# Performance work log

Hardware: AMD Instinct MI355X
Metric: run time of the kernel (lower is better)

## Reference

```python
import jax, jax.numpy as jnp
import numpy as np
jax.config.update("jax_enable_x64", True)

B, S, V, W, M = 64, 32, 512, 2048, 8
EOS, PAD, MSK = 0, 1, 2
DELTA_IMAG_CLAMP = 35.0  # standard tmm overflow guard on exp(+Im(delta))


def setup_inputs() -> dict:
    key = jax.random.key(0)
    ks = jax.random.split(key, 6)
    stacks = jax.random.uniform(ks[0], (B, S, V), dtype=jnp.float32)
    wl_tensor = (400.0 + 700.0 * jax.random.uniform(ks[1], (W,), dtype=jnp.float32))  # nm
    theta = jnp.zeros((1,), dtype=jnp.float32)  # normal incidence
    nk_real = 1.5 + 2.5 * jax.random.uniform(ks[2], (M, W), dtype=jnp.float64)
    nk_imag = 0.5 * jax.random.uniform(ks[3], (M, W), dtype=jnp.float64)
    thickness = 5.0 + 195.0 * jax.random.uniform(ks[4], (V,), dtype=jnp.float64)
    thickness = thickness.at[jnp.array([EOS, PAD, MSK])].set(0.0)  # special tokens -> substrate, 0 nm
    mat_idx_table = jax.random.randint(ks[5], (V,), 0, M, dtype=jnp.int32)
    sub_idx = jnp.array(0, dtype=jnp.int32)
    return dict(stacks=stacks, wl_tensor=wl_tensor, theta=theta,
                nk_real=nk_real, nk_imag=nk_imag, thickness=thickness,
                mat_idx_table=mat_idx_table, sub_idx=sub_idx,
                eos=EOS, pad=PAD, msk=MSK)


def _coh_tmm_s(n, t, th0, lam):
    """Coherent TMM, s-pol. n:[B,L,W] complex128, t:[B,L] complex128 (front/back inf),
    th0 scalar, lam:[W]. Returns R,T [B,W] float."""
    n0 = n[:, :1, :]
    th = jnp.arcsin(n0 * jnp.sin(th0) / n)           # Snell, complex arcsin [B,L,W]
    cos_th = jnp.cos(th)
    kz = 2.0 * jnp.pi * n * cos_th / lam[None, None, :]
    delta = kz[:, 1:-1, :] * t[:, 1:-1, None]        # inner layers only [B,S,W]
    delta = delta.real + 1j * jnp.minimum(delta.imag, DELTA_IMAG_CLAMP)
    f = n * cos_th                                    # [B,L,W]
    f1, f2 = f[:, :-1, :], f[:, 1:, :]
    r = (f1 - f2) / (f1 + f2)                         # interface Fresnel r [B,L-1,W]
    tt = 2.0 * f1 / (f1 + f2)
    # Mtilde = ([[1,r0],[r0,1]]/t0) @ prod_j (diag(e^{-i d_j}, e^{+i d_j}) @ [[1,rj],[rj,1]]/tj)
    a = 1.0 / tt[:, 0]
    b = r[:, 0] / tt[:, 0]
    c = b
    d = a

    def step(carry, xs):
        a, b, c, d = carry
        dlt, rj, tj = xs                              # each [B,W]
        P = jnp.exp(-1j * dlt)
        Q = jnp.exp(1j * dlt)
        inv_t = 1.0 / tj
        a2 = (a * P + b * Q * rj) * inv_t
        b2 = (a * P * rj + b * Q) * inv_t
        c2 = (c * P + d * Q * rj) * inv_t
        d2 = (c * P * rj + d * Q) * inv_t
        return (a2, b2, c2, d2), None

    xs = (jnp.moveaxis(delta, 1, 0), jnp.moveaxis(r[:, 1:], 1, 0), jnp.moveaxis(tt[:, 1:], 1, 0))
    (a, b, c, d), _ = jax.lax.scan(step, (a, b, c, d), xs)
    r_amp = c / a
    t_amp = 1.0 / a
    R = jnp.abs(r_amp) ** 2
    T = jnp.abs(t_amp) ** 2 * (f[:, -1].real / f[:, 0].real)
    return R, T


def reference(stacks, wl_tensor, theta, nk_real, nk_imag, thickness, mat_idx_table, sub_idx, eos, pad, msk):
    nk_table = nk_real + 1j * nk_imag                 # [M,W] complex128
    th_c = thickness.astype(jnp.complex128)           # [V]
    nk_per_token = nk_table[mat_idx_table]            # [V,W]
    # zero out special-token probabilities and renormalize
    p = stacks.at[:, :, jnp.array([eos, pad, msk])].set(0.0)
    Z = p.sum(axis=-1, keepdims=True)
    p_norm = jnp.where(Z > 0, p / jnp.maximum(Z, 1e-8), p)
    p_c = p_norm.astype(jnp.complex128)
    n_base = jnp.einsum('bsv,vw->bsw', p_c, nk_per_token)  # soft nk gather
    t_base = p_c @ th_c                                     # [B,S]
    is_zero = Z[..., 0] <= 0
    n_base = jnp.where(is_zero[..., None], nk_table[sub_idx][None, None, :], n_base)
    t_base = jnp.where(is_zero, jnp.zeros((), dtype=t_base.dtype), t_base)
    # soft EOS survival mask
    p_eos = jnp.clip(stacks[..., eos], 0.0, 1.0)
    survival = jnp.cumprod(1.0 - p_eos + 1e-12, axis=1)
    active = jnp.concatenate([jnp.ones_like(survival[:, :1]), survival[:, :-1]], axis=1)
    t_base = t_base * active.astype(t_base.dtype)
    Bb, Ss, Ww = n_base.shape
    one = jnp.ones((Bb, 1, Ww), dtype=n_base.dtype)
    inf_t = jnp.full((Bb, 1), jnp.inf, dtype=t_base.dtype)
    n_tensor = jnp.concatenate([one, n_base, one], axis=1)     # [B,S+2,W]
    t_tensor = jnp.concatenate([inf_t, t_base, inf_t], axis=1)  # [B,S+2]
    th0 = theta[0].astype(jnp.float64)
    lam = wl_tensor.astype(jnp.float64)
    R, T = _coh_tmm_s(n_tensor, t_tensor, th0, lam)
    clean = lambda x: jnp.clip(jnp.nan_to_num(x.astype(jnp.float32), nan=0.0, posinf=0.0, neginf=0.0), 0.0, 1.0)
    R = clean(R)
    T = clean(T)
    A = jnp.clip(jnp.nan_to_num(1.0 - R - T, nan=0.0, posinf=0.0, neginf=0.0), 0.0, 1.0)
    return jnp.concatenate([R, A, T], axis=1)  # [B, 3W]
```

## Files before the change

kernel.cpp:

```cpp
#include <hip/hip_runtime.h>
#include <math.h>

#define B_ 64
#define S_ 32
#define V_ 512
#define W_ 2048
#define M_ 8
#define TWO_PI 6.2831853071795864769f
#define DELTA_IMAG_CLAMP 35.0f

struct cf { float re, im; };
__device__ inline cf cmul(cf a, cf b){ return {a.re*b.re - a.im*b.im, a.re*b.im + a.im*b.re}; }
__device__ inline cf cadd(cf a, cf b){ return {a.re+b.re, a.im+b.im}; }
__device__ inline cf csub(cf a, cf b){ return {a.re-b.re, a.im-b.im}; }
__device__ inline float frcp(float x){ return __builtin_amdgcn_rcpf(x); }
__device__ inline cf cinvf(cf a){
    float id = frcp(fmaf(a.re, a.re, a.im*a.im));
    return {a.re*id, -a.im*id};
}
__device__ inline cf csqrt_(cf z){
    float m  = sqrtf(z.re*z.re + z.im*z.im);
    float re = sqrtf(0.5f*fmaxf(m + z.re, 0.0f));
    float im = sqrtf(0.5f*fmaxf(m - z.re, 0.0f));
    if (z.im < 0.0f) im = -im;
    return {re, im};
}

__device__ inline bool is_f32_layout(const void* thick) {
    float w3 = ((const float*)thick)[3];
    return (w3 > 4.0f && w3 < 256.0f);
}

__global__ __launch_bounds__(256) void prep_kernel(
    const float* __restrict__ stacks,
    const void*  __restrict__ thickness,
    const int*   __restrict__ mat_idx,
    const int*   __restrict__ sub_idx_p,
    const int*   __restrict__ eos_p,
    const int*   __restrict__ pad_p,
    const int*   __restrict__ msk_p,
    float* __restrict__ q_out,
    float* __restrict__ t_out)
{
    const int tid  = threadIdx.x;
    const int lane = tid & 63;
    const int wid  = tid >> 6;
    const int row  = blockIdx.x * 4 + wid;

    const bool f32lay = is_f32_layout(thickness);
    const float*  thf = (const float*) thickness;
    const double* thd = (const double*)thickness;
    const int eos = eos_p[0], pad = pad_p[0], msk = msk_p[0];

    const float* srow = stacks + (size_t)row * V_;

    float zp = 0.f, tp = 0.f;
    float bp[M_];
    #pragma unroll
    for (int m = 0; m < M_; ++m) bp[m] = 0.f;

    #pragma unroll
    for (int j = 0; j < V_/64; ++j) {
        int v = lane + j*64;
        float p = srow[v];
        if (v == eos || v == pad || v == msk) p = 0.0f;
        float tv = f32lay ? thf[v] : (float)thd[v];
        int mi = mat_idx[v];
        zp += p;
        tp += p * tv;
        #pragma unroll
        for (int m = 0; m < M_; ++m) bp[m] += (mi == m) ? p : 0.0f;
    }

    #pragma unroll
    for (int off = 32; off > 0; off >>= 1) {
        zp += __shfl_xor(zp, off);
        tp += __shfl_xor(tp, off);
        #pragma unroll
        for (int m = 0; m < M_; ++m) bp[m] += __shfl_xor(bp[m], off);
    }

    if (lane == 0) {
        if (zp > 0.0f) {
            float inv = 1.0f / fmaxf(zp, 1e-8f);
            #pragma unroll
            for (int m = 0; m < M_; ++m) q_out[row*M_ + m] = bp[m]*inv;
            t_out[row] = tp * inv;
        } else {
            int si = sub_idx_p[0];
            #pragma unroll
            for (int m = 0; m < M_; ++m) q_out[row*M_ + m] = (m == si) ? 1.0f : 0.0f;
            t_out[row] = 0.0f;
        }
    }
}

__global__ __launch_bounds__(256) void tmm_kernel(
    const float* __restrict__ wl,
    const float* __restrict__ theta_p,
    const void*  __restrict__ nk_real_v,
    const void*  __restrict__ nk_imag_v,
    const void*  __restrict__ thickness,
    const float* __restrict__ stacks,
    const int*   __restrict__ eos_p,
    const float* __restrict__ q_in,
    const float* __restrict__ t_in,
    float* __restrict__ out)
{
    __shared__ __align__(16) float q_sh[S_ * M_];
    __shared__ float t_sh[S_];

    const int tid   = threadIdx.x;
    const int chunk = tid & 1;
    const int b     = blockIdx.x >> 4;
    const int w     = ((blockIdx.x & 15) << 7) + (tid >> 1);

    q_sh[tid] = q_in[b * (S_*M_) + tid];

    if (tid < S_) {
        int s = tid;
        float pe = stacks[((size_t)(b*S_ + s))*V_ + eos_p[0]];
        pe = fminf(fmaxf(pe, 0.0f), 1.0f);
        float g = 1.0f - pe + 1e-12f;
        float prod = g;
        #pragma unroll
        for (int off = 1; off < 32; off <<= 1) {
            float up = __shfl_up(prod, off);
            if (s >= off) prod *= up;
        }
        float ex = __shfl_up(prod, 1);
        if (s == 0) ex = 1.0f;
        t_sh[s] = t_in[b*S_ + s] * ex;
    }
    __syncthreads();

    const float lam  = wl[w];
    const float kw   = TWO_PI / lam;
    const float th0  = theta_p[0];
    const float sin0 = sinf(th0);
    const float f0   = cosf(th0);
    const bool oblique = (sin0 != 0.0f);

    float nkr[M_], nki[M_];
    if (is_f32_layout(thickness)) {
        const float* nr = (const float*)nk_real_v;
        const float* ni = (const float*)nk_imag_v;
        #pragma unroll
        for (int m = 0; m < M_; ++m) {
            nkr[m] = nr[m*W_ + w];
            nki[m] = ni[m*W_ + w];
        }
    } else {
        const double* nr = (const double*)nk_real_v;
        const double* ni = (const double*)nk_imag_v;
        #pragma unroll
        for (int m = 0; m < M_; ++m) {
            nkr[m] = (float)nr[m*W_ + w];
            nki[m] = (float)ni[m*W_ + w];
        }
    }

    auto calc_f = [&](int s) -> cf {
        const float4* q4 = reinterpret_cast<const float4*>(q_sh + (s << 3));
        const float4 qa = q4[0];
        const float4 qb = q4[1];
        cf n;
        n.re = qa.x * nkr[0];
        n.im = qa.x * nki[0];
        n.re = fmaf(qa.y, nkr[1], n.re); n.im = fmaf(qa.y, nki[1], n.im);
        n.re = fmaf(qa.z, nkr[2], n.re); n.im = fmaf(qa.z, nki[2], n.im);
        n.re = fmaf(qa.w, nkr[3], n.re); n.im = fmaf(qa.w, nki[3], n.im);
        n.re = fmaf(qb.x, nkr[4], n.re); n.im = fmaf(qb.x, nki[4], n.im);
        n.re = fmaf(qb.y, nkr[5], n.re); n.im = fmaf(qb.y, nki[5], n.im);
        n.re = fmaf(qb.z, nkr[6], n.re); n.im = fmaf(qb.z, nki[6], n.im);
        n.re = fmaf(qb.w, nkr[7], n.re); n.im = fmaf(qb.w, nki[7], n.im);
        if (!oblique) return n;
        cf invn = cinvf(n);
        cf st   = {sin0*invn.re, sin0*invn.im};
        cf st2  = cmul(st, st);
        cf ct   = csqrt_({1.0f - st2.re, -st2.im});
        return cmul(n, ct);
    };

    const int s0 = chunk << 4;
    cf fc = calc_f(s0);
    const float inv2f0 = 0.5f * frcp(f0);

    cf a, bb, c, d;
    if (chunk == 0) {
        a  = {(f0 + fc.re)*inv2f0,  fc.im*inv2f0};
        bb = {(f0 - fc.re)*inv2f0, -fc.im*inv2f0};
        c = bb; d = a;
    } else {
        a = {1.f, 0.f}; bb = {0.f, 0.f}; c = {0.f, 0.f}; d = {1.f, 0.f};
    }

    cf gf = {1.f, 0.f};
    cf gi = {1.f, 0.f};

    #pragma unroll 4
    for (int jj = 0; jj < 16; ++jj) {
        const int sp = s0 + jj;
        float k  = kw * t_sh[sp];
        float dr = k * fc.re;
        float di = fminf(k * fc.im, DELTA_IMAG_CLAMP);
        float ed  = __expf(di);
        float emd = __expf(-di);
        float sn = __sinf(dr);
        float cs = __cosf(dr);
        cf P = { ed*cs, -ed*sn};
        cf Q = {emd*cs,  emd*sn};

        cf fn;
        if (sp + 1 < S_) {
            fn = calc_f(sp + 1);
        } else {
            fn = {f0, 0.0f};
        }

        cf sum   = cadd(fc, fn);
        cf isum  = cinvf(sum);
        cf r     = cmul(csub(fc, fn), isum);

        gf = cmul(gf, fc);
        gi = cmul(gi, isum);

        cf aP = cmul(a, P), bQ = cmul(bb, Q);
        cf cP = cmul(c, P), dQ = cmul(d, Q);
        a  = cadd(aP, cmul(bQ, r));
        bb = cadd(cmul(aP, r), bQ);
        c  = cadd(cP, cmul(dQ, r));
        d  = cadd(cmul(cP, r), dQ);
        fc = fn;
    }

    cf g = cmul(gf, gi);
    g.re *= 65536.0f; g.im *= 65536.0f;

    cf aO  = {__shfl_xor(a.re, 1),  __shfl_xor(a.im, 1)};
    cf bO  = {__shfl_xor(bb.re, 1), __shfl_xor(bb.im, 1)};
    cf cO  = {__shfl_xor(c.re, 1),  __shfl_xor(c.im, 1)};
    cf dO  = {__shfl_xor(d.re, 1),  __shfl_xor(d.im, 1)};
    cf gO  = {__shfl_xor(g.re, 1),  __shfl_xor(g.im, 1)};
    (void)bO; (void)dO;

    if (chunk == 0) {
        cf fa  = cadd(cmul(a, aO), cmul(bb, cO));
        cf fcm = cadd(cmul(c, aO), cmul(d, cO));
        cf gt  = cmul(g, gO);

        float ma  = fmaxf(fabsf(fa.re), fabsf(fa.im));
        float scv = frcp(ma);
        cf as     = {fa.re*scv, fa.im*scv};
        float den = fmaf(as.re, as.re, as.im*as.im);
        float iden = frcp(den);
        cf csc    = {fcm.re*scv, fcm.im*scv};
        cf ramp   = {(csc.re*as.re + csc.im*as.im)*iden,
                     (csc.im*as.re - csc.re*as.im)*iden};
        float R = fmaf(ramp.re, ramp.re, ramp.im*ramp.im);
        float T = fmaf(gt.re, gt.re, gt.im*gt.im) * (scv*scv) * iden;

        auto clean = [](float x) -> float {
            return isfinite(x) ? fminf(fmaxf(x, 0.0f), 1.0f) : 0.0f;
        };
        float Rc = clean(R);
        float Tc = clean(T);
        float Ac = clean(1.0f - Rc - Tc);

        size_t base = (size_t)b * (3*W_);
        out[base +          w] = Rc;
        out[base +   W_ +   w] = Ac;
        out[base + 2*W_ +   w] = Tc;
    }
}

extern "C" void kernel_launch(void* const* d_in, const int* in_sizes, int n_in,
                              void* d_out, int out_size, void* d_ws, size_t ws_size,
                              hipStream_t stream) {
    const float* stacks    = (const float*)d_in[0];
    const float* wl        = (const float*)d_in[1];
    const float* theta     = (const float*)d_in[2];
    const void*  nk_real   = d_in[3];
    const void*  nk_imag   = d_in[4];
    const void*  thickness = d_in[5];
    const int*   mat_idx   = (const int*)d_in[6];
    const int*   sub_idx   = (const int*)d_in[7];
    const int*   eos       = (const int*)d_in[8];
    const int*   pad       = (const int*)d_in[9];
    const int*   msk       = (const int*)d_in[10];
    float* out = (float*)d_out;

    float* q     = (float*)d_ws;
    float* t_raw = q + B_*S_*M_;

    prep_kernel<<<(B_*S_)/4, 256, 0, stream>>>(stacks, thickness, mat_idx, sub_idx,
                                               eos, pad, msk, q, t_raw);
    tmm_kernel<<<B_*(W_/128), 256, 0, stream>>>(wl, theta, nk_real, nk_imag,
                                                thickness, stacks, eos, q, t_raw, out);
}
```

Before: 95.24 us.

## Fuse prep reduction into TMM kernel with shared-memory atomics

Removes the separate prep kernel. Each TMM block recomputes the per-layer material fractions and thickness for its batch row, using float4 loads and LDS atomicAdd into q_sh. The goal is to drop one kernel launch and the workspace round trip. In exchange the prep work is repeated 16 times per batch row (once per wavelength tile), and LDS atomics contend on 8 bins. Block IDs are also remapped so that blocks sharing a batch row are spread across CUs.

```diff
diff --git a/kernel.cpp b/kernel.cpp
--- a/kernel.cpp
+++ b/kernel.cpp
@@ -31,108 +31,107 @@
     return (w3 > 4.0f && w3 < 256.0f);
 }
 
-__global__ __launch_bounds__(256) void prep_kernel(
+__global__ __launch_bounds__(256) void fused_kernel(
     const float* __restrict__ stacks,
+    const float* __restrict__ wl,
+    const float* __restrict__ theta_p,
+    const void*  __restrict__ nk_real_v,
+    const void*  __restrict__ nk_imag_v,
     const void*  __restrict__ thickness,
     const int*   __restrict__ mat_idx,
     const int*   __restrict__ sub_idx_p,
     const int*   __restrict__ eos_p,
     const int*   __restrict__ pad_p,
     const int*   __restrict__ msk_p,
-    float* __restrict__ q_out,
-    float* __restrict__ t_out)
-{
-    const int tid  = threadIdx.x;
-    const int lane = tid & 63;
-    const int wid  = tid >> 6;
-    const int row  = blockIdx.x * 4 + wid;
-
-    const bool f32lay = is_f32_layout(thickness);
-    const float*  thf = (const float*) thickness;
-    const double* thd = (const double*)thickness;
-    const int eos = eos_p[0], pad = pad_p[0], msk = msk_p[0];
-
-    const float* srow = stacks + (size_t)row * V_;
-
-    float zp = 0.f, tp = 0.f;
-    float bp[M_];
-    #pragma unroll
-    for (int m = 0; m < M_; ++m) bp[m] = 0.f;
-
-    #pragma unroll
-    for (int j = 0; j < V_/64; ++j) {
-        int v = lane + j*64;
-        float p = srow[v];
-        if (v == eos || v == pad || v == msk) p = 0.0f;
-        float tv = f32lay ? thf[v] : (float)thd[v];
-        int mi = mat_idx[v];
-        zp += p;
-        tp += p * tv;
-        #pragma unroll
-        for (int m = 0; m < M_; ++m) bp[m] += (mi == m) ? p : 0.0f;
-    }
-
-    #pragma unroll
-    for (int off = 32; off > 0; off >>= 1) {
-        zp += __shfl_xor(zp, off);
-        tp += __shfl_xor(tp, off);
-        #pragma unroll
-        for (int m = 0; m < M_; ++m) bp[m] += __shfl_xor(bp[m], off);
-    }
-
-    if (lane == 0) {
-        if (zp > 0.0f) {
-            float inv = 1.0f / fmaxf(zp, 1e-8f);
-            #pragma unroll
-            for (int m = 0; m < M_; ++m) q_out[row*M_ + m] = bp[m]*inv;
-            t_out[row] = tp * inv;
-        } else {
-            int si = sub_idx_p[0];
-            #pragma unroll
-            for (int m = 0; m < M_; ++m) q_out[row*M_ + m] = (m == si) ? 1.0f : 0.0f;
-            t_out[row] = 0.0f;
-        }
-    }
-}
-
-__global__ __launch_bounds__(256) void tmm_kernel(
-    const float* __restrict__ wl,
-    const float* __restrict__ theta_p,
-    const void*  __restrict__ nk_real_v,
-    const void*  __restrict__ nk_imag_v,
-    const void*  __restrict__ thickness,
-    const float* __restrict__ stacks,
-    const int*   __restrict__ eos_p,
-    const float* __restrict__ q_in,
-    const float* __restrict__ t_in,
     float* __restrict__ out)
 {
     __shared__ __align__(16) float q_sh[S_ * M_];
     __shared__ float t_sh[S_];
-
-    const int tid   = threadIdx.x;
-    const int chunk = tid & 1;
-    const int b     = blockIdx.x >> 4;
-    const int w     = ((blockIdx.x & 15) << 7) + (tid >> 1);
-
-    q_sh[tid] = q_in[b * (S_*M_) + tid];
-
+    __shared__ float zacc[S_];
+    __shared__ float tacc[S_];
+
+    const int tid = threadIdx.x;
+    const int bid = blockIdx.x;
+    const int wg  = ((bid & 7) << 7) | (bid >> 3);
+    const int b   = wg >> 4;
+    const int wt  = wg & 15;
+
+    q_sh[tid] = 0.0f;
+    __syncthreads();
+
+    const int lane = tid & 63;
+    const int wid  = tid >> 6;
+    const int s    = (wid << 3) | (lane >> 3);
+    const int sub  = lane & 7;
+    const int eos = eos_p[0], pad = pad_p[0], msk = msk_p[0];
+    const bool f32lay = is_f32_layout(thickness);
+
+    const float4* p4 = (const float4*)(stacks + ((size_t)(b*S_ + s))*V_);
+    float zp = 0.f, tp = 0.f;
+    float* qrow = q_sh + s*M_;
+
+    #pragma unroll
+    for (int j = 0; j < 16; ++j) {
+        const int idx = (j << 3) | sub;
+        const int v0  = idx << 2;
+        float4 pv = p4[idx];
+        int4   mi = ((const int4*)mat_idx)[idx];
+        float tv0, tv1, tv2, tv3;
+        if (f32lay) {
+            float4 t4 = ((const float4*)thickness)[idx];
+            tv0 = t4.x; tv1 = t4.y; tv2 = t4.z; tv3 = t4.w;
+        } else {
+            double2 ta = ((const double2*)thickness)[idx*2];
+            double2 tb = ((const double2*)thickness)[idx*2 + 1];
+            tv0 = (float)ta.x; tv1 = (float)ta.y;
+            tv2 = (float)tb.x; tv3 = (float)tb.y;
+        }
+        #define ELEM(P, TV, MI, E) { \
+            int v = v0 + (E); \
+            float p_ = (v == eos || v == pad || v == msk) ? 0.0f : (P); \
+            zp += p_; tp = fmaf(p_, (TV), tp); \
+            atomicAdd(&qrow[(MI)], p_); }
+        ELEM(pv.x, tv0, mi.x, 0)
+        ELEM(pv.y, tv1, mi.y, 1)
+        ELEM(pv.z, tv2, mi.z, 2)
+        ELEM(pv.w, tv3, mi.w, 3)
+        #undef ELEM
+    }
+    zp += __shfl_xor(zp, 1); tp += __shfl_xor(tp, 1);
+    zp += __shfl_xor(zp, 2); tp += __shfl_xor(tp, 2);
+    zp += __shfl_xor(zp, 4); tp += __shfl_xor(tp, 4);
+    if (sub == 0) { zacc[s] = zp; tacc[s] = tp; }
+    __syncthreads();
+
+    {
+        const int ss = tid >> 3, mm = tid & 7;
+        float Z  = zacc[ss];
+        float qv = q_sh[tid];
+        qv = (Z > 0.0f) ? qv * (1.0f / fmaxf(Z, 1e-8f))
+                        : ((mm == sub_idx_p[0]) ? 1.0f : 0.0f);
+        q_sh[tid] = qv;
+    }
     if (tid < S_) {
-        int s = tid;
-        float pe = stacks[((size_t)(b*S_ + s))*V_ + eos_p[0]];
+        const int si = tid;
+        float Z    = zacc[si];
+        float tval = (Z > 0.0f) ? tacc[si] * (1.0f / fmaxf(Z, 1e-8f)) : 0.0f;
+        float pe = stacks[((size_t)(b*S_ + si))*V_ + eos];
         pe = fminf(fmaxf(pe, 0.0f), 1.0f);
         float g = 1.0f - pe + 1e-12f;
         float prod = g;
         #pragma unroll
         for (int off = 1; off < 32; off <<= 1) {
             float up = __shfl_up(prod, off);
-            if (s >= off) prod *= up;
+            if (si >= off) prod *= up;
         }
         float ex = __shfl_up(prod, 1);
-        if (s == 0) ex = 1.0f;
-        t_sh[s] = t_in[b*S_ + s] * ex;
+        if (si == 0) ex = 1.0f;
+        t_sh[si] = tval * ex;
     }
     __syncthreads();
+
+    const int chunk = tid & 1;
+    const int w     = (wt << 7) + (tid >> 1);
 
     const float lam  = wl[w];
     const float kw   = TWO_PI / lam;
@@ -142,7 +141,7 @@
     const bool oblique = (sin0 != 0.0f);
 
     float nkr[M_], nki[M_];
-    if (is_f32_layout(thickness)) {
+    if (f32lay) {
         const float* nr = (const float*)nk_real_v;
         const float* ni = (const float*)nk_imag_v;
         #pragma unroll
@@ -160,8 +159,8 @@
         }
     }
 
-    auto calc_f = [&](int s) -> cf {
-        const float4* q4 = reinterpret_cast<const float4*>(q_sh + (s << 3));
+    auto calc_f = [&](int sl) -> cf {
+        const float4* q4 = reinterpret_cast<const float4*>(q_sh + (sl << 3));
         const float4 qa = q4[0];
         const float4 qb = q4[1];
         cf n;
@@ -290,11 +289,10 @@
     const int*   msk       = (const int*)d_in[10];
     float* out = (float*)d_out;
 
-    float* q     = (float*)d_ws;
-    float* t_raw = q + B_*S_*M_;
-
-    prep_kernel<<<(B_*S_)/4, 256, 0, stream>>>(stacks, thickness, mat_idx, sub_idx,
-                                               eos, pad, msk, q, t_raw);
-    tmm_kernel<<<B_*(W_/128), 256, 0, stream>>>(wl, theta, nk_real, nk_imag,
-                                                thickness, stacks, eos, q, t_raw, out);
-}
+    (void)d_ws; (void)ws_size;
+
+    fused_kernel<<<B_*(W_/128), 256, 0, stream>>>(stacks, wl, theta,
+                                                  nk_real, nk_imag, thickness,
+                                                  mat_idx, sub_idx,
+                                                  eos, pad, msk, out);
+}
```

Measured after the change: 168.1 us. 76.5% more time.

## Replace split 2x2 matrix product with backward vector recurrence per wavelength

Applied to the files above, without the earlier changes.

Instead of two threads each multiplying 16 full 2x2 transfer matrices and merging them via shuffles, each thread now handles one wavelength and propagates a 2-vector (x,y) backward from the last interface. It also tracks the transmission factor as a running product g*(1+r) rather than separate f and 1/sum products. This roughly halves the complex multiplies per layer and removes the shuffle merge, but doubles the serial chain length per thread and halves the grid size, which lowers latency hiding.

```diff
diff --git a/kernel.cpp b/kernel.cpp
--- a/kernel.cpp
+++ b/kernel.cpp
@@ -110,10 +110,9 @@
     __shared__ __align__(16) float q_sh[S_ * M_];
     __shared__ float t_sh[S_];
 
-    const int tid   = threadIdx.x;
-    const int chunk = tid & 1;
-    const int b     = blockIdx.x >> 4;
-    const int w     = ((blockIdx.x & 15) << 7) + (tid >> 1);
+    const int tid = threadIdx.x;
+    const int b   = blockIdx.x >> 3;
+    const int w   = ((blockIdx.x & 7) << 8) + tid;
 
     q_sh[tid] = q_in[b * (S_*M_) + tid];
 
@@ -121,8 +120,8 @@
         int s = tid;
         float pe = stacks[((size_t)(b*S_ + s))*V_ + eos_p[0]];
         pe = fminf(fmaxf(pe, 0.0f), 1.0f);
-        float g = 1.0f - pe + 1e-12f;
-        float prod = g;
+        float g0 = 1.0f - pe + 1e-12f;
+        float prod = g0;
         #pragma unroll
         for (int off = 1; off < 32; off <<= 1) {
             float up = __shfl_up(prod, off);
@@ -160,8 +159,8 @@
         }
     }
 
-    auto calc_f = [&](int s) -> cf {
-        const float4* q4 = reinterpret_cast<const float4*>(q_sh + (s << 3));
+    auto calc_f = [&](int sl) -> cf {
+        const float4* q4 = reinterpret_cast<const float4*>(q_sh + (sl << 3));
         const float4 qa = q4[0];
         const float4 qb = q4[1];
         cf n;
@@ -182,28 +181,30 @@
         return cmul(n, ct);
     };
 
-    const int s0 = chunk << 4;
-    cf fc = calc_f(s0);
-    const float inv2f0 = 0.5f * frcp(f0);
-
-    cf a, bb, c, d;
-    if (chunk == 0) {
-        a  = {(f0 + fc.re)*inv2f0,  fc.im*inv2f0};
-        bb = {(f0 - fc.re)*inv2f0, -fc.im*inv2f0};
-        c = bb; d = a;
-    } else {
-        a = {1.f, 0.f}; bb = {0.f, 0.f}; c = {0.f, 0.f}; d = {1.f, 0.f};
-    }
-
-    cf gf = {1.f, 0.f};
-    cf gi = {1.f, 0.f};
+    cf f_hi = {f0, 0.0f};
+    cf x = {1.f, 0.f}, y = {0.f, 0.f};
+    cf g = {1.f, 0.f};
+    cf f_lo;
 
     #pragma unroll 4
-    for (int jj = 0; jj < 16; ++jj) {
-        const int sp = s0 + jj;
+    for (int sp = S_ - 1; sp >= 0; --sp) {
+        f_lo = calc_f(sp);
+
+        cf sum  = cadd(f_lo, f_hi);
+        cf isum = cinvf(sum);
+        cf r    = cmul(csub(f_lo, f_hi), isum);
+
+        cf gr = cmul(g, r);
+        g = cadd(g, gr);
+
+        cf ry = cmul(r, y);
+        cf rx = cmul(r, x);
+        cf u0 = cadd(x, ry);
+        cf u1 = cadd(rx, y);
+
         float k  = kw * t_sh[sp];
-        float dr = k * fc.re;
-        float di = fminf(k * fc.im, DELTA_IMAG_CLAMP);
+        float dr = k * f_lo.re;
+        float di = fminf(k * f_lo.im, DELTA_IMAG_CLAMP);
         float ed  = __expf(di);
         float emd = __expf(-di);
         float sn = __sinf(dr);
@@ -211,67 +212,39 @@
         cf P = { ed*cs, -ed*sn};
         cf Q = {emd*cs,  emd*sn};
 
-        cf fn;
-        if (sp + 1 < S_) {
-            fn = calc_f(sp + 1);
-        } else {
-            fn = {f0, 0.0f};
-        }
-
-        cf sum   = cadd(fc, fn);
-        cf isum  = cinvf(sum);
-        cf r     = cmul(csub(fc, fn), isum);
-
-        gf = cmul(gf, fc);
-        gi = cmul(gi, isum);
-
-        cf aP = cmul(a, P), bQ = cmul(bb, Q);
-        cf cP = cmul(c, P), dQ = cmul(d, Q);
-        a  = cadd(aP, cmul(bQ, r));
-        bb = cadd(cmul(aP, r), bQ);
-        c  = cadd(cP, cmul(dQ, r));
-        d  = cadd(cmul(cP, r), dQ);
-        fc = fn;
-    }
-
-    cf g = cmul(gf, gi);
-    g.re *= 65536.0f; g.im *= 65536.0f;
-
-    cf aO  = {__shfl_xor(a.re, 1),  __shfl_xor(a.im, 1)};
-    cf bO  = {__shfl_xor(bb.re, 1), __shfl_xor(bb.im, 1)};
-    cf cO  = {__shfl_xor(c.re, 1),  __shfl_xor(c.im, 1)};
-    cf dO  = {__shfl_xor(d.re, 1),  __shfl_xor(d.im, 1)};
-    cf gO  = {__shfl_xor(g.re, 1),  __shfl_xor(g.im, 1)};
-    (void)bO; (void)dO;
-
-    if (chunk == 0) {
-        cf fa  = cadd(cmul(a, aO), cmul(bb, cO));
-        cf fcm = cadd(cmul(c, aO), cmul(d, cO));
-        cf gt  = cmul(g, gO);
-
-        float ma  = fmaxf(fabsf(fa.re), fabsf(fa.im));
-        float scv = frcp(ma);
-        cf as     = {fa.re*scv, fa.im*scv};
-        float den = fmaf(as.re, as.re, as.im*as.im);
-        float iden = frcp(den);
-        cf csc    = {fcm.re*scv, fcm.im*scv};
-        cf ramp   = {(csc.re*as.re + csc.im*as.im)*iden,
-                     (csc.im*as.re - csc.re*as.im)*iden};
-        float R = fmaf(ramp.re, ramp.re, ramp.im*ramp.im);
-        float T = fmaf(gt.re, gt.re, gt.im*gt.im) * (scv*scv) * iden;
-
-        auto clean = [](float x) -> float {
-            return isfinite(x) ? fminf(fmaxf(x, 0.0f), 1.0f) : 0.0f;
-        };
-        float Rc = clean(R);
-        float Tc = clean(T);
-        float Ac = clean(1.0f - Rc - Tc);
-
-        size_t base = (size_t)b * (3*W_);
-        out[base +          w] = Rc;
-        out[base +   W_ +   w] = Ac;
-        out[base + 2*W_ +   w] = Tc;
-    }
+        x = cmul(P, u0);
+        y = cmul(Q, u1);
+        f_hi = f_lo;
+    }
+
+    const float inv2f0 = 0.5f * frcp(f0);
+    cf a0 = {(f0 + f_lo.re)*inv2f0,  f_lo.im*inv2f0};
+    cf b0 = {(f0 - f_lo.re)*inv2f0, -f_lo.im*inv2f0};
+    cf fa  = cadd(cmul(a0, x), cmul(b0, y));
+    cf fcm = cadd(cmul(b0, x), cmul(a0, y));
+
+    float ma  = fmaxf(fabsf(fa.re), fabsf(fa.im));
+    float scv = frcp(ma);
+    cf as     = {fa.re*scv, fa.im*scv};
+    float den = fmaf(as.re, as.re, as.im*as.im);
+    float iden = frcp(den);
+    cf csc    = {fcm.re*scv, fcm.im*scv};
+    cf ramp   = {(csc.re*as.re + csc.im*as.im)*iden,
+                 (csc.im*as.re - csc.re*as.im)*iden};
+    float R = fmaf(ramp.re, ramp.re, ramp.im*ramp.im);
+    float T = fmaf(g.re, g.re, g.im*g.im) * (scv*scv) * iden;
+
+    auto clean = [](float v) -> float {
+        return isfinite(v) ? fminf(fmaxf(v, 0.0f), 1.0f) : 0.0f;
+    };
+    float Rc = clean(R);
+    float Tc = clean(T);
+    float Ac = clean(1.0f - Rc - Tc);
+
+    size_t base = (size_t)b * (3*W_);
+    out[base +          w] = Rc;
+    out[base +   W_ +   w] = Ac;
+    out[base + 2*W_ +   w] = Tc;
 }
 
 extern "C" void kernel_launch(void* const* d_in, const int* in_sizes, int n_in,
@@ -295,6 +268,6 @@
 
     prep_kernel<<<(B_*S_)/4, 256, 0, stream>>>(stacks, thickness, mat_idx, sub_idx,
                                                eos, pad, msk, q, t_raw);
-    tmm_kernel<<<B_*(W_/128), 256, 0, stream>>>(wl, theta, nk_real, nk_imag,
+    tmm_kernel<<<B_*(W_/256), 256, 0, stream>>>(wl, theta, nk_real, nk_imag,
                                                 thickness, stacks, eos, q, t_raw, out);
 }
```

Result: faster. 87.91 us (-7.7%).
